# Kernel optimization log

Measured on AMD Instinct MI355X. Metric: run time of the kernel, lower is better.

The kernel has to match this reference:

```python
import jax, jax.numpy as jnp
import numpy as np

B, CE, CD = 4, 128, 256
HE = WE = 256
HD = WD = 128
N = CE // 8  # 16


def _up2_align_corners(x):
    # bilinear upsample x2 with align_corners=True (matches nn.UpsamplingBilinear2d)
    def axis_up(x, axis, n_in):
        n_out = 2 * n_in
        pos = jnp.arange(n_out, dtype=x.dtype) * ((n_in - 1) / (n_out - 1))
        i0 = jnp.clip(jnp.floor(pos).astype(jnp.int32), 0, n_in - 1)
        i1 = jnp.clip(i0 + 1, 0, n_in - 1)
        w = pos - i0.astype(x.dtype)
        shape = [1] * x.ndim
        shape[axis] = n_out
        w = w.reshape(shape)
        return jnp.take(x, i0, axis=axis) * (1 - w) + jnp.take(x, i1, axis=axis) * w
    x = axis_up(x, 2, x.shape[2])
    return axis_up(x, 3, x.shape[3])


def _conv7(x, w, b):
    y = jax.lax.conv_general_dilated(x, w, (1, 1), [(3, 3), (3, 3)],
                                     dimension_numbers=('NCHW', 'OIHW', 'NCHW'))
    return y + b.reshape(1, -1, 1, 1)


def _sag_branch(x, w1, b1, w2, b2):
    mx = jnp.max(x, axis=1, keepdims=True)           # channel max-pool [B,1,H,W]
    av = jnp.mean(x, axis=1, keepdims=True)          # channel avg-pool
    c1 = jnp.einsum('bchw,oc->bohw', x, w1) + b1.reshape(1, -1, 1, 1)  # 1x1 conv -> 1 ch
    return _conv7(jnp.concatenate([mx, av, c1], axis=1), w2, b2)       # [B,1,H,W]


def _cag_branch(x, wa, ba, wm, bm):
    av = jnp.mean(x, axis=(2, 3))                    # [B,C] global avg
    mx = jnp.max(x, axis=(2, 3))                     # [B,C] global max
    return av @ wa.T + ba + mx @ wm.T + bm           # [B,N]


def setup_inputs() -> dict:
    key = jax.random.key(0)
    ks = jax.random.split(key, 20)
    s = 0.02
    return {
        'x_enc': jax.random.normal(ks[0], (B, CE, HE, WE), jnp.float32),
        'x_dec': jax.random.normal(ks[1], (B, CD, HD, WD), jnp.float32),
        'cw_ea': jax.random.normal(ks[2], (N, CE), jnp.float32) * s,
        'cb_ea': jnp.zeros((N,), jnp.float32),
        'cw_em': jax.random.normal(ks[3], (N, CE), jnp.float32) * s,
        'cb_em': jnp.zeros((N,), jnp.float32),
        'cw_da': jax.random.normal(ks[4], (N, CD), jnp.float32) * s,
        'cb_da': jnp.zeros((N,), jnp.float32),
        'cw_dm': jax.random.normal(ks[5], (N, CD), jnp.float32) * s,
        'cb_dm': jnp.zeros((N,), jnp.float32),
        'cw_f': jax.random.normal(ks[6], (CE, N), jnp.float32) * s,
        'cb_f': jnp.zeros((CE,), jnp.float32),
        'sw1_e': jax.random.normal(ks[7], (1, CE), jnp.float32) * s,
        'sb1_e': jnp.zeros((1,), jnp.float32),
        'sw2_e': jax.random.normal(ks[8], (1, 3, 7, 7), jnp.float32) * s,
        'sb2_e': jnp.zeros((1,), jnp.float32),
        'sw1_d': jax.random.normal(ks[9], (1, CD), jnp.float32) * s,
        'sb1_d': jnp.zeros((1,), jnp.float32),
        'sw2_d': jax.random.normal(ks[10], (1, 3, 7, 7), jnp.float32) * s,
        'sb2_d': jnp.zeros((1,), jnp.float32),
        'save_attention': 0,
    }


def reference(x_enc, x_dec, cw_ea, cb_ea, cw_em, cb_em, cw_da, cb_da, cw_dm, cb_dm,
              cw_f, cb_f, sw1_e, sb1_e, sw2_e, sb2_e, sw1_d, sb1_d, sw2_d, sb2_d,
              save_attention):
    # decoder path: upsample x2 (align_corners=True) + ReLU
    dec_feat = jax.nn.relu(_up2_align_corners(x_dec))  # [B,CD,2HD,2WD]
    # encoder path: center crop to match
    h2, w2 = 2 * x_dec.shape[2], 2 * x_dec.shape[3]
    s0 = (x_enc.shape[2] - h2) // 2
    s1 = (x_enc.shape[3] - w2) // 2
    enc_feat = x_enc[:, :, s0:s0 + h2, s1:s1 + w2]
    # spatial attention gate (sAG)
    spat = jax.nn.sigmoid(_sag_branch(enc_feat, sw1_e, sb1_e, sw2_e, sb2_e)
                          + _sag_branch(dec_feat, sw1_d, sb1_d, sw2_d, sb2_d))  # [B,1,H,W]
    # channel attention gate (cAG)
    ce = _cag_branch(enc_feat, cw_ea, cb_ea, cw_em, cb_em)  # [B,N]
    cd = _cag_branch(dec_feat, cw_da, cb_da, cw_dm, cb_dm)  # [B,N]
    ch = jax.nn.sigmoid((ce + cd) @ cw_f.T + cb_f)           # [B,CE]
    return enc_feat * spat * ch[:, :, None, None]
```

## Files before the change

kernel.cpp:

```cpp
#include <hip/hip_runtime.h>
#include <math.h>

static const int B_  = 4;
static const int CE_ = 128;
static const int CD_ = 256;
static const int HE_ = 256;
static const int HD_ = 128;
static const int N_  = 16;
#define PLANE  65536
#define DPLANE 16384
#define UPSCALE (127.0f/255.0f)

__global__ __launch_bounds__(256) void k_stats(
    const float* __restrict__ xe, const float* __restrict__ xd,
    const float* __restrict__ sw1e, const float* __restrict__ sb1e,
    const float* __restrict__ sw1d, const float* __restrict__ sb1d,
    float* __restrict__ stats, float* __restrict__ eav, float* __restrict__ emx,
    float* __restrict__ dav, float* __restrict__ dmx) {
  __shared__ float smem[512];
  int blk = blockIdx.x;
  int t = threadIdx.x;

  if (blk < 1024) {
    int b = blk >> 8, h = blk & 255;
    float bias = sb1e[0];
    if (t < CE_) smem[t] = sw1e[t];
    __syncthreads();
    const float* base = xe + (((size_t)b * CE_) * HE_ + h) * (size_t)HE_ + t;
    float mx = -INFINITY, sm = 0.f, pj = 0.f;
#pragma unroll 4
    for (int c = 0; c < CE_; ++c) {
      float v = base[(size_t)c * PLANE];
      mx = fmaxf(mx, v);
      sm += v;
      pj = fmaf(v, smem[c], pj);
    }
    size_t o = (((size_t)b * 6) * HE_ + h) * (size_t)HE_ + t;
    stats[o] = mx;
    stats[o + (size_t)PLANE] = sm * (1.f / CE_);
    stats[o + 2 * (size_t)PLANE] = pj + bias;

  } else if (blk < 1536) {
    int bc = blk - 1024;
    const float4* p = (const float4*)(xe + (size_t)bc * PLANE);
    float sm = 0.f, m = -INFINITY;
    for (int i = t; i < PLANE / 4; i += 256) {
      float4 v = p[i];
      sm += (v.x + v.y) + (v.z + v.w);
      m = fmaxf(m, fmaxf(fmaxf(v.x, v.y), fmaxf(v.z, v.w)));
    }
    float* ss = smem;
    float* sx = smem + 256;
    ss[t] = sm; sx[t] = m;
    __syncthreads();
    for (int s = 128; s > 0; s >>= 1) {
      if (t < s) { ss[t] += ss[t + s]; sx[t] = fmaxf(sx[t], sx[t + s]); }
      __syncthreads();
    }
    if (t == 0) { eav[bc] = ss[0] * (1.f / PLANE); emx[bc] = sx[0]; }

  } else if (blk < 2560) {
    int bh = blk - 1536;
    int b = bh >> 8, h = bh & 255;
    float bias = sb1d[0];
    smem[t] = sw1d[t];
    __syncthreads();
    float ph = (float)h * UPSCALE;
    int ih0 = (int)ph; float wh = ph - (float)ih0;
    int ih1 = min(ih0 + 1, HD_ - 1);
    float pw = (float)t * UPSCALE;
    int iw0 = (int)pw; float ww = pw - (float)iw0;
    int iw1 = min(iw0 + 1, HD_ - 1);
    float w00 = (1.f - wh) * (1.f - ww), w01 = (1.f - wh) * ww;
    float w10 = wh * (1.f - ww),        w11 = wh * ww;
    const float* xb = xd + (size_t)b * CD_ * DPLANE;
    int o00 = ih0 * HD_ + iw0, o01 = ih0 * HD_ + iw1;
    int o10 = ih1 * HD_ + iw0, o11 = ih1 * HD_ + iw1;
    float mx = -INFINITY, sm = 0.f, pj = 0.f;
#pragma unroll 2
    for (int c = 0; c < CD_; ++c) {
      const float* pc = xb + (size_t)c * DPLANE;
      float v = w00 * pc[o00] + w01 * pc[o01] + w10 * pc[o10] + w11 * pc[o11];
      v = fmaxf(v, 0.f);
      mx = fmaxf(mx, v);
      sm += v;
      pj = fmaf(v, smem[c], pj);
    }
    size_t o = (((size_t)b * 6 + 3) * HE_ + h) * (size_t)HE_ + t;
    stats[o] = mx;
    stats[o + (size_t)PLANE] = sm * (1.f / CD_);
    stats[o + 2 * (size_t)PLANE] = pj + bias;

  } else {
    int bc = blk - 2560;
    const float* p = xd + (size_t)bc * DPLANE;
    float pw = (float)t * UPSCALE;
    int iw0 = (int)pw; float ww = pw - (float)iw0;
    int iw1 = min(iw0 + 1, HD_ - 1);
    float sm = 0.f, m = -INFINITY;
#pragma unroll 4
    for (int hh = 0; hh < 256; ++hh) {
      float ph = (float)hh * UPSCALE;
      int ih0 = (int)ph; float wh = ph - (float)ih0;
      int ih1 = min(ih0 + 1, HD_ - 1);
      const float* r0 = p + ih0 * HD_;
      const float* r1 = p + ih1 * HD_;
      float top = r0[iw0] * (1.f - ww) + r0[iw1] * ww;
      float bot = r1[iw0] * (1.f - ww) + r1[iw1] * ww;
      float v = fmaxf((1.f - wh) * top + wh * bot, 0.f);
      sm += v;
      m = fmaxf(m, v);
    }
    float* ss = smem;
    float* sx = smem + 256;
    ss[t] = sm; sx[t] = m;
    __syncthreads();
    for (int s = 128; s > 0; s >>= 1) {
      if (t < s) { ss[t] += ss[t + s]; sx[t] = fmaxf(sx[t], sx[t + s]); }
      __syncthreads();
    }
    if (t == 0) { dav[bc] = ss[0] * (1.f / PLANE); dmx[bc] = sx[0]; }
  }
}

__global__ __launch_bounds__(256) void k_gate(
    const float* __restrict__ stats,
    const float* __restrict__ we, const float* __restrict__ be,
    const float* __restrict__ wd, const float* __restrict__ bd,
    const float* __restrict__ eav, const float* __restrict__ emx,
    const float* __restrict__ dav, const float* __restrict__ dmx,
    const float* __restrict__ cw_ea, const float* __restrict__ cb_ea,
    const float* __restrict__ cw_em, const float* __restrict__ cb_em,
    const float* __restrict__ cw_da, const float* __restrict__ cb_da,
    const float* __restrict__ cw_dm, const float* __restrict__ cb_dm,
    const float* __restrict__ cw_f, const float* __restrict__ cb_f,
    const float* __restrict__ x, float* __restrict__ out) {
  int bh = blockIdx.x;
  int b = bh >> 8, h = bh & 255;
  int t = threadIdx.x;
  int w = t;

  __shared__ float swE[147], swD[147];
  __shared__ float part[16][17];
  __shared__ float s_n[16];
  __shared__ float s_ch[128];
  __shared__ float s_spat[256];

  if (t < 147) { swE[t] = we[t]; swD[t] = wd[t]; }

  {
    int n = t & 15, sl = t >> 4;
    const float* ea = eav + b * CE_;
    const float* em = emx + b * CE_;
    const float* da = dav + b * CD_;
    const float* dm = dmx + b * CD_;
    float p = 0.f;
#pragma unroll
    for (int i = 0; i < 8; ++i) {
      int c = sl * 8 + i;
      p = fmaf(ea[c], cw_ea[n * CE_ + c], p);
      p = fmaf(em[c], cw_em[n * CE_ + c], p);
    }
#pragma unroll
    for (int i = 0; i < 16; ++i) {
      int c = sl * 16 + i;
      p = fmaf(da[c], cw_da[n * CD_ + c], p);
      p = fmaf(dm[c], cw_dm[n * CD_ + c], p);
    }
    part[n][sl] = p;
  }
  __syncthreads();
  if (t < 16) {
    float s = cb_ea[t] + cb_em[t] + cb_da[t] + cb_dm[t];
#pragma unroll
    for (int sl = 0; sl < 16; ++sl) s += part[t][sl];
    s_n[t] = s;
  }
  __syncthreads();
  if (t < 128) {
    float s = cb_f[t];
#pragma unroll
    for (int n = 0; n < N_; ++n) s = fmaf(s_n[n], cw_f[t * N_ + n], s);
    s_ch[t] = 1.f / (1.f + __expf(-s));
  }

  float acc = be[0] + bd[0];
  const float* sb = stats + ((size_t)b * 6) * PLANE;
#pragma unroll
  for (int ic = 0; ic < 3; ++ic) {
    const float* pe = sb + (size_t)ic * PLANE;
    const float* pd = sb + (size_t)(ic + 3) * PLANE;
#pragma unroll
    for (int ky = 0; ky < 7; ++ky) {
      int y = h + ky - 3;
      if ((unsigned)y >= 256u) continue;
      const float* rowE = pe + y * 256;
      const float* rowD = pd + y * 256;
#pragma unroll
      for (int kx = 0; kx < 7; ++kx) {
        int xw = w + kx - 3;
        if ((unsigned)xw >= 256u) continue;
        float we_ = swE[ic * 49 + ky * 7 + kx];
        float wd_ = swD[ic * 49 + ky * 7 + kx];
        acc = fmaf(rowE[xw], we_, acc);
        acc = fmaf(rowD[xw], wd_, acc);
      }
    }
  }
  s_spat[w] = 1.f / (1.f + __expf(-acc));
  __syncthreads();

  int w4 = t & 63;
  int cq = t >> 6;
  float4 sv = ((const float4*)s_spat)[w4];
  const float4* xp = (const float4*)x + ((size_t)b * CE_) * (PLANE / 4) + h * 64;
  float4*       op = (float4*)out     + ((size_t)b * CE_) * (PLANE / 4) + h * 64;
  for (int c = cq; c < CE_; c += 4) {
    float cv = s_ch[c];
    float4 xv = xp[(size_t)c * (PLANE / 4) + w4];
    float4 o;
    o.x = xv.x * sv.x * cv;
    o.y = xv.y * sv.y * cv;
    o.z = xv.z * sv.z * cv;
    o.w = xv.w * sv.w * cv;
    op[(size_t)c * (PLANE / 4) + w4] = o;
  }
}

extern "C" void kernel_launch(void* const* d_in, const int* in_sizes, int n_in,
                              void* d_out, int out_size, void* d_ws, size_t ws_size,
                              hipStream_t stream) {
  const float* x_enc = (const float*)d_in[0];
  const float* x_dec = (const float*)d_in[1];
  const float* cw_ea = (const float*)d_in[2];
  const float* cb_ea = (const float*)d_in[3];
  const float* cw_em = (const float*)d_in[4];
  const float* cb_em = (const float*)d_in[5];
  const float* cw_da = (const float*)d_in[6];
  const float* cb_da = (const float*)d_in[7];
  const float* cw_dm = (const float*)d_in[8];
  const float* cb_dm = (const float*)d_in[9];
  const float* cw_f  = (const float*)d_in[10];
  const float* cb_f  = (const float*)d_in[11];
  const float* sw1_e = (const float*)d_in[12];
  const float* sb1_e = (const float*)d_in[13];
  const float* sw2_e = (const float*)d_in[14];
  const float* sb2_e = (const float*)d_in[15];
  const float* sw1_d = (const float*)d_in[16];
  const float* sb1_d = (const float*)d_in[17];
  const float* sw2_d = (const float*)d_in[18];
  const float* sb2_d = (const float*)d_in[19];
  float* out = (float*)d_out;
  (void)in_sizes; (void)n_in; (void)out_size; (void)ws_size;

  float* ws    = (float*)d_ws;
  float* stats = ws;
  float* eav   = ws + 1572864;
  float* emx   = eav + 512;
  float* dav   = emx + 512;
  float* dmx   = dav + 1024;

  k_stats<<<3584, 256, 0, stream>>>(x_enc, x_dec, sw1_e, sb1_e, sw1_d, sb1_d,
                                    stats, eav, emx, dav, dmx);
  k_gate <<<B_ * HE_, 256, 0, stream>>>(stats, sw2_e, sb2_e, sw2_d, sb2_d,
                                        eav, emx, dav, dmx,
                                        cw_ea, cb_ea, cw_em, cb_em,
                                        cw_da, cb_da, cw_dm, cb_dm,
                                        cw_f, cb_f, x_enc, out);
}
```

Before: 455.1 us.

## Fuse encoder global avg/max pooling into per-pixel channel stats via atomics

Removes the separate pass that re-read every encoder plane for global average and max. The per-pixel channel-reduction blocks now use float4 loads and do wave reductions per channel, pushing partial sums and max keys to global memory with atomicAdd and atomicMax on order-preserving unsigned keys. A memset zeroes the accumulators, and the decoder plane pass precomputes row offsets and weights in shared memory. The cost is many atomics and shuffle reductions inside the channel loop, and float atomic summation becomes nondeterministic.

Measured after the change: 646.2 us. 42.0% more time.

```diff
diff --git a/kernel.cpp b/kernel.cpp
--- a/kernel.cpp
+++ b/kernel.cpp
@@ -11,57 +11,27 @@
 #define DPLANE 16384
 #define UPSCALE (127.0f/255.0f)
 
+__device__ __forceinline__ unsigned fkey(float f) {
+  unsigned b = __float_as_uint(f);
+  return (b & 0x80000000u) ? ~b : (b | 0x80000000u);
+}
+__device__ __forceinline__ float fdec(unsigned k) {
+  return __uint_as_float((k & 0x80000000u) ? (k & 0x7fffffffu) : ~k);
+}
+
 __global__ __launch_bounds__(256) void k_stats(
     const float* __restrict__ xe, const float* __restrict__ xd,
     const float* __restrict__ sw1e, const float* __restrict__ sb1e,
     const float* __restrict__ sw1d, const float* __restrict__ sb1d,
-    float* __restrict__ stats, float* __restrict__ eav, float* __restrict__ emx,
+    float* __restrict__ stats, float* __restrict__ eav_sum,
+    unsigned* __restrict__ emx_key,
     float* __restrict__ dav, float* __restrict__ dmx) {
-  __shared__ float smem[512];
+  __shared__ float smem[768];
   int blk = blockIdx.x;
   int t = threadIdx.x;
 
   if (blk < 1024) {
     int b = blk >> 8, h = blk & 255;
-    float bias = sb1e[0];
-    if (t < CE_) smem[t] = sw1e[t];
-    __syncthreads();
-    const float* base = xe + (((size_t)b * CE_) * HE_ + h) * (size_t)HE_ + t;
-    float mx = -INFINITY, sm = 0.f, pj = 0.f;
-#pragma unroll 4
-    for (int c = 0; c < CE_; ++c) {
-      float v = base[(size_t)c * PLANE];
-      mx = fmaxf(mx, v);
-      sm += v;
-      pj = fmaf(v, smem[c], pj);
-    }
-    size_t o = (((size_t)b * 6) * HE_ + h) * (size_t)HE_ + t;
-    stats[o] = mx;
-    stats[o + (size_t)PLANE] = sm * (1.f / CE_);
-    stats[o + 2 * (size_t)PLANE] = pj + bias;
-
-  } else if (blk < 1536) {
-    int bc = blk - 1024;
-    const float4* p = (const float4*)(xe + (size_t)bc * PLANE);
-    float sm = 0.f, m = -INFINITY;
-    for (int i = t; i < PLANE / 4; i += 256) {
-      float4 v = p[i];
-      sm += (v.x + v.y) + (v.z + v.w);
-      m = fmaxf(m, fmaxf(fmaxf(v.x, v.y), fmaxf(v.z, v.w)));
-    }
-    float* ss = smem;
-    float* sx = smem + 256;
-    ss[t] = sm; sx[t] = m;
-    __syncthreads();
-    for (int s = 128; s > 0; s >>= 1) {
-      if (t < s) { ss[t] += ss[t + s]; sx[t] = fmaxf(sx[t], sx[t + s]); }
-      __syncthreads();
-    }
-    if (t == 0) { eav[bc] = ss[0] * (1.f / PLANE); emx[bc] = sx[0]; }
-
-  } else if (blk < 2560) {
-    int bh = blk - 1536;
-    int b = bh >> 8, h = bh & 255;
     float bias = sb1d[0];
     smem[t] = sw1d[t];
     __syncthreads();
@@ -77,7 +47,7 @@
     int o00 = ih0 * HD_ + iw0, o01 = ih0 * HD_ + iw1;
     int o10 = ih1 * HD_ + iw0, o11 = ih1 * HD_ + iw1;
     float mx = -INFINITY, sm = 0.f, pj = 0.f;
-#pragma unroll 2
+#pragma unroll 4
     for (int c = 0; c < CD_; ++c) {
       const float* pc = xb + (size_t)c * DPLANE;
       float v = w00 * pc[o00] + w01 * pc[o01] + w10 * pc[o10] + w11 * pc[o11];
@@ -91,26 +61,36 @@
     stats[o + (size_t)PLANE] = sm * (1.f / CD_);
     stats[o + 2 * (size_t)PLANE] = pj + bias;
 
-  } else {
-    int bc = blk - 2560;
+  } else if (blk < 2048) {
+    int bc = blk - 1024;
     const float* p = xd + (size_t)bc * DPLANE;
+    int*   so0  = (int*)smem;
+    int*   so1  = so0 + 256;
+    float* swht = smem + 512;
+    {
+      float ph = (float)t * UPSCALE;
+      int ih0 = (int)ph;
+      so0[t]  = ih0 * HD_;
+      so1[t]  = min(ih0 + 1, HD_ - 1) * HD_;
+      swht[t] = ph - (float)ih0;
+    }
     float pw = (float)t * UPSCALE;
     int iw0 = (int)pw; float ww = pw - (float)iw0;
     int iw1 = min(iw0 + 1, HD_ - 1);
+    __syncthreads();
     float sm = 0.f, m = -INFINITY;
 #pragma unroll 4
     for (int hh = 0; hh < 256; ++hh) {
-      float ph = (float)hh * UPSCALE;
-      int ih0 = (int)ph; float wh = ph - (float)ih0;
-      int ih1 = min(ih0 + 1, HD_ - 1);
-      const float* r0 = p + ih0 * HD_;
-      const float* r1 = p + ih1 * HD_;
+      const float* r0 = p + so0[hh];
+      const float* r1 = p + so1[hh];
+      float wh = swht[hh];
       float top = r0[iw0] * (1.f - ww) + r0[iw1] * ww;
       float bot = r1[iw0] * (1.f - ww) + r1[iw1] * ww;
       float v = fmaxf((1.f - wh) * top + wh * bot, 0.f);
       sm += v;
       m = fmaxf(m, v);
     }
+    __syncthreads();
     float* ss = smem;
     float* sx = smem + 256;
     ss[t] = sm; sx[t] = m;
@@ -120,6 +100,52 @@
       __syncthreads();
     }
     if (t == 0) { dav[bc] = ss[0] * (1.f / PLANE); dmx[bc] = sx[0]; }
+
+  } else {
+    int bb = blk - 2048;
+    int b = bb >> 6;
+    int h0 = (bb & 63) * 4;
+    int r = t >> 6, q = t & 63;
+    int h = h0 + r;
+    float bias = sb1e[0];
+    if (t < CE_) smem[t] = sw1e[t];
+    __syncthreads();
+    const float4* base = (const float4*)xe + (size_t)(b * CE_) * (PLANE / 4)
+                         + (size_t)h * 64 + q;
+    float4 mx4 = make_float4(-INFINITY, -INFINITY, -INFINITY, -INFINITY);
+    float4 sm4 = make_float4(0.f, 0.f, 0.f, 0.f);
+    float4 pj4 = make_float4(0.f, 0.f, 0.f, 0.f);
+    float* eacc = eav_sum + b * CE_;
+    unsigned* emk = emx_key + b * CE_;
+#pragma unroll 4
+    for (int c = 0; c < CE_; ++c) {
+      float4 v = base[(size_t)c * (PLANE / 4)];
+      float wc = smem[c];
+      mx4.x = fmaxf(mx4.x, v.x); mx4.y = fmaxf(mx4.y, v.y);
+      mx4.z = fmaxf(mx4.z, v.z); mx4.w = fmaxf(mx4.w, v.w);
+      sm4.x += v.x; sm4.y += v.y; sm4.z += v.z; sm4.w += v.w;
+      pj4.x = fmaf(v.x, wc, pj4.x); pj4.y = fmaf(v.y, wc, pj4.y);
+      pj4.z = fmaf(v.z, wc, pj4.z); pj4.w = fmaf(v.w, wc, pj4.w);
+      float cs = (v.x + v.y) + (v.z + v.w);
+      float cm = fmaxf(fmaxf(v.x, v.y), fmaxf(v.z, v.w));
+#pragma unroll
+      for (int msk = 32; msk > 0; msk >>= 1) {
+        cs += __shfl_xor(cs, msk);
+        cm = fmaxf(cm, __shfl_xor(cm, msk));
+      }
+      if ((t & 63) == 0) {
+        atomicAdd(&eacc[c], cs);
+        atomicMax(&emk[c], fkey(cm));
+      }
+    }
+    size_t o4 = (size_t)(b * 6) * (PLANE / 4) + (size_t)h * 64 + q;
+    float4* so = (float4*)stats;
+    so[o4] = mx4;
+    sm4.x *= (1.f / CE_); sm4.y *= (1.f / CE_);
+    sm4.z *= (1.f / CE_); sm4.w *= (1.f / CE_);
+    so[o4 + PLANE / 4] = sm4;
+    pj4.x += bias; pj4.y += bias; pj4.z += bias; pj4.w += bias;
+    so[o4 + 2 * (PLANE / 4)] = pj4;
   }
 }
 
@@ -127,7 +153,7 @@
     const float* __restrict__ stats,
     const float* __restrict__ we, const float* __restrict__ be,
     const float* __restrict__ wd, const float* __restrict__ bd,
-    const float* __restrict__ eav, const float* __restrict__ emx,
+    const float* __restrict__ eav_sum, const unsigned* __restrict__ emx_key,
     const float* __restrict__ dav, const float* __restrict__ dmx,
     const float* __restrict__ cw_ea, const float* __restrict__ cb_ea,
     const float* __restrict__ cw_em, const float* __restrict__ cb_em,
@@ -150,16 +176,16 @@
 
   {
     int n = t & 15, sl = t >> 4;
-    const float* ea = eav + b * CE_;
-    const float* em = emx + b * CE_;
+    const float* ea = eav_sum + b * CE_;
+    const unsigned* ek = emx_key + b * CE_;
     const float* da = dav + b * CD_;
     const float* dm = dmx + b * CD_;
     float p = 0.f;
 #pragma unroll
     for (int i = 0; i < 8; ++i) {
       int c = sl * 8 + i;
-      p = fmaf(ea[c], cw_ea[n * CE_ + c], p);
-      p = fmaf(em[c], cw_em[n * CE_ + c], p);
+      p = fmaf(ea[c] * (1.f / PLANE), cw_ea[n * CE_ + c], p);
+      p = fmaf(fdec(ek[c]), cw_em[n * CE_ + c], p);
     }
 #pragma unroll
     for (int i = 0; i < 16; ++i) {
@@ -255,12 +281,14 @@
 
   float* ws    = (float*)d_ws;
   float* stats = ws;
-  float* eav   = ws + 1572864;
-  float* emx   = eav + 512;
-  float* dav   = emx + 512;
-  float* dmx   = dav + 1024;
-
-  k_stats<<<3584, 256, 0, stream>>>(x_enc, x_dec, sw1_e, sb1_e, sw1_d, sb1_d,
+  float*    eav = ws + 1572864;
+  unsigned* emx = (unsigned*)(ws + 1573376);
+  float*    dav = ws + 1573888;
+  float*    dmx = ws + 1574912;
+
+  hipMemsetAsync(eav, 0, 1024 * sizeof(float), stream);
+
+  k_stats<<<2304, 256, 0, stream>>>(x_enc, x_dec, sw1_e, sb1_e, sw1_d, sb1_d,
                                     stats, eav, emx, dav, dmx);
   k_gate <<<B_ * HE_, 256, 0, stream>>>(stats, sw2_e, sb2_e, sw2_d, sb2_d,
                                         eav, emx, dav, dmx,
```

## Vectorize encoder stats, stage decoder rows in LDS, precompute upsample row tables

Applied to the files above, without the earlier changes.

The encoder per-pixel stats loop now reads float4 and splits the channel loop across four thread groups, then combines the partials with a shared-memory reduction so that loads are wider. The decoder per-pixel branch stages the two needed source rows of each channel into double-buffered LDS with a register prefetch, replacing four scattered global gathers per channel. The price is a __syncthreads on every channel iteration. The decoder global-pool branch precomputes row offsets and weights into shared memory instead of recomputing them on every iteration.

Measured after the change: 438.7 us. 3.6% less time.

```diff
diff --git a/kernel.cpp b/kernel.cpp
--- a/kernel.cpp
+++ b/kernel.cpp
@@ -11,34 +11,61 @@
 #define DPLANE 16384
 #define UPSCALE (127.0f/255.0f)
 
+__device__ __forceinline__ float4 fmax4(float4 a, float4 b) {
+  return make_float4(fmaxf(a.x, b.x), fmaxf(a.y, b.y), fmaxf(a.z, b.z), fmaxf(a.w, b.w));
+}
+__device__ __forceinline__ float4 fadd4(float4 a, float4 b) {
+  return make_float4(a.x + b.x, a.y + b.y, a.z + b.z, a.w + b.w);
+}
+
 __global__ __launch_bounds__(256) void k_stats(
     const float* __restrict__ xe, const float* __restrict__ xd,
     const float* __restrict__ sw1e, const float* __restrict__ sb1e,
     const float* __restrict__ sw1d, const float* __restrict__ sb1d,
     float* __restrict__ stats, float* __restrict__ eav, float* __restrict__ emx,
     float* __restrict__ dav, float* __restrict__ dmx) {
-  __shared__ float smem[512];
+  __shared__ float smem[1024];
+  __shared__ float4 red[3][256];
   int blk = blockIdx.x;
   int t = threadIdx.x;
 
   if (blk < 1024) {
     int b = blk >> 8, h = blk & 255;
+    int cs = t >> 6, q = t & 63;
     float bias = sb1e[0];
     if (t < CE_) smem[t] = sw1e[t];
     __syncthreads();
-    const float* base = xe + (((size_t)b * CE_) * HE_ + h) * (size_t)HE_ + t;
-    float mx = -INFINITY, sm = 0.f, pj = 0.f;
+    const float4* base = (const float4*)xe + (size_t)b * CE_ * (PLANE / 4)
+                         + (size_t)h * 64 + q;
+    float4 mx4 = make_float4(-INFINITY, -INFINITY, -INFINITY, -INFINITY);
+    float4 sm4 = make_float4(0.f, 0.f, 0.f, 0.f);
+    float4 pj4 = make_float4(0.f, 0.f, 0.f, 0.f);
 #pragma unroll 4
-    for (int c = 0; c < CE_; ++c) {
-      float v = base[(size_t)c * PLANE];
-      mx = fmaxf(mx, v);
-      sm += v;
-      pj = fmaf(v, smem[c], pj);
-    }
-    size_t o = (((size_t)b * 6) * HE_ + h) * (size_t)HE_ + t;
-    stats[o] = mx;
-    stats[o + (size_t)PLANE] = sm * (1.f / CE_);
-    stats[o + 2 * (size_t)PLANE] = pj + bias;
+    for (int c = cs; c < CE_; c += 4) {
+      float4 v = base[(size_t)c * (PLANE / 4)];
+      float wc = smem[c];
+      mx4 = fmax4(mx4, v);
+      sm4 = fadd4(sm4, v);
+      pj4.x = fmaf(v.x, wc, pj4.x); pj4.y = fmaf(v.y, wc, pj4.y);
+      pj4.z = fmaf(v.z, wc, pj4.z); pj4.w = fmaf(v.w, wc, pj4.w);
+    }
+    red[0][t] = mx4; red[1][t] = sm4; red[2][t] = pj4;
+    __syncthreads();
+    if (t < 64) {
+      float4 m = fmax4(fmax4(red[0][t], red[0][t + 64]),
+                       fmax4(red[0][t + 128], red[0][t + 192]));
+      float4 s = fadd4(fadd4(red[1][t], red[1][t + 64]),
+                       fadd4(red[1][t + 128], red[1][t + 192]));
+      float4 p = fadd4(fadd4(red[2][t], red[2][t + 64]),
+                       fadd4(red[2][t + 128], red[2][t + 192]));
+      float4* so = (float4*)stats;
+      size_t o4 = (size_t)(b * 6) * (PLANE / 4) + (size_t)h * 64 + t;
+      so[o4] = m;
+      s.x *= (1.f / CE_); s.y *= (1.f / CE_); s.z *= (1.f / CE_); s.w *= (1.f / CE_);
+      so[o4 + PLANE / 4] = s;
+      p.x += bias; p.y += bias; p.z += bias; p.w += bias;
+      so[o4 + 2 * (PLANE / 4)] = p;
+    }
 
   } else if (blk < 1536) {
     int bc = blk - 1024;
@@ -63,28 +90,34 @@
     int bh = blk - 1536;
     int b = bh >> 8, h = bh & 255;
     float bias = sb1d[0];
-    smem[t] = sw1d[t];
-    __syncthreads();
+    float* swt  = smem;
+    float* buf0 = smem + 256;
+    float* buf1 = smem + 512;
+    swt[t] = sw1d[t];
     float ph = (float)h * UPSCALE;
     int ih0 = (int)ph; float wh = ph - (float)ih0;
     int ih1 = min(ih0 + 1, HD_ - 1);
+    int rowoff = (ih1 - ih0) * HD_;
     float pw = (float)t * UPSCALE;
     int iw0 = (int)pw; float ww = pw - (float)iw0;
     int iw1 = min(iw0 + 1, HD_ - 1);
-    float w00 = (1.f - wh) * (1.f - ww), w01 = (1.f - wh) * ww;
-    float w10 = wh * (1.f - ww),        w11 = wh * ww;
-    const float* xb = xd + (size_t)b * CD_ * DPLANE;
-    int o00 = ih0 * HD_ + iw0, o01 = ih0 * HD_ + iw1;
-    int o10 = ih1 * HD_ + iw0, o11 = ih1 * HD_ + iw1;
+    const float* xb = xd + (size_t)b * CD_ * DPLANE + ih0 * HD_;
+    int li = min(t, DPLANE - ih0 * HD_ - 1);
+    float pre = xb[li];
     float mx = -INFINITY, sm = 0.f, pj = 0.f;
-#pragma unroll 2
     for (int c = 0; c < CD_; ++c) {
-      const float* pc = xb + (size_t)c * DPLANE;
-      float v = w00 * pc[o00] + w01 * pc[o01] + w10 * pc[o10] + w11 * pc[o11];
-      v = fmaxf(v, 0.f);
+      float* bw = (c & 1) ? buf1 : buf0;
+      bw[t] = pre;
+      if (c + 1 < CD_) pre = xb[(size_t)(c + 1) * DPLANE + li];
+      __syncthreads();
+      float l00 = bw[iw0], l01 = bw[iw1];
+      float l10 = bw[rowoff + iw0], l11 = bw[rowoff + iw1];
+      float top = l00 + ww * (l01 - l00);
+      float bot = l10 + ww * (l11 - l10);
+      float v = fmaxf(top + wh * (bot - top), 0.f);
       mx = fmaxf(mx, v);
       sm += v;
-      pj = fmaf(v, smem[c], pj);
+      pj = fmaf(v, swt[c], pj);
     }
     size_t o = (((size_t)b * 6 + 3) * HE_ + h) * (size_t)HE_ + t;
     stats[o] = mx;
@@ -94,23 +127,33 @@
   } else {
     int bc = blk - 2560;
     const float* p = xd + (size_t)bc * DPLANE;
+    int*   so0  = (int*)smem;
+    int*   so1  = so0 + 256;
+    float* swht = smem + 512;
+    {
+      float ph = (float)t * UPSCALE;
+      int ih0 = (int)ph;
+      so0[t]  = ih0 * HD_;
+      so1[t]  = min(ih0 + 1, HD_ - 1) * HD_;
+      swht[t] = ph - (float)ih0;
+    }
     float pw = (float)t * UPSCALE;
     int iw0 = (int)pw; float ww = pw - (float)iw0;
     int iw1 = min(iw0 + 1, HD_ - 1);
+    __syncthreads();
     float sm = 0.f, m = -INFINITY;
 #pragma unroll 4
     for (int hh = 0; hh < 256; ++hh) {
-      float ph = (float)hh * UPSCALE;
-      int ih0 = (int)ph; float wh = ph - (float)ih0;
-      int ih1 = min(ih0 + 1, HD_ - 1);
-      const float* r0 = p + ih0 * HD_;
-      const float* r1 = p + ih1 * HD_;
+      const float* r0 = p + so0[hh];
+      const float* r1 = p + so1[hh];
+      float wh = swht[hh];
       float top = r0[iw0] * (1.f - ww) + r0[iw1] * ww;
       float bot = r1[iw0] * (1.f - ww) + r1[iw1] * ww;
       float v = fmaxf((1.f - wh) * top + wh * bot, 0.f);
       sm += v;
       m = fmaxf(m, v);
     }
+    __syncthreads();
     float* ss = smem;
     float* sx = smem + 256;
     ss[t] = sm; sx[t] = m;
```
